# Kernel optimization log

Measured on AMD Instinct MI355X. Metric: run time of the kernel, lower is better.

Reference implementation:

```python
import jax, jax.numpy as jnp
import numpy as np

D_MODEL = 1024
NUM_HEADS = 16
D_K = D_MODEL // NUM_HEADS


def setup_inputs() -> dict:
    key = jax.random.key(0)
    ks = jax.random.split(key, 13)
    B, S = 2, 2048
    s = 1.0 / np.sqrt(D_MODEL)
    inp = {
        'q': jax.random.normal(ks[0], (B, S, D_MODEL), jnp.float32),
        'k': jax.random.normal(ks[1], (B, S, D_MODEL), jnp.float32),
        'v': jax.random.normal(ks[2], (B, S, D_MODEL), jnp.float32),
        'mask': jax.random.randint(ks[3], (B, S), 0, 2, jnp.int32),
        'Wq': jax.random.normal(ks[4], (D_MODEL, D_MODEL), jnp.float32) * s,
        'bq': jax.random.normal(ks[5], (D_MODEL,), jnp.float32) * s,
        'Wk': jax.random.normal(ks[6], (D_MODEL, D_MODEL), jnp.float32) * s,
        'bk': jax.random.normal(ks[7], (D_MODEL,), jnp.float32) * s,
        'Wv': jax.random.normal(ks[8], (D_MODEL, D_MODEL), jnp.float32) * s,
        'bv': jax.random.normal(ks[9], (D_MODEL,), jnp.float32) * s,
        'Wo': jax.random.normal(ks[10], (D_MODEL, D_MODEL), jnp.float32) * s,
        'bo': jax.random.normal(ks[11], (D_MODEL,), jnp.float32) * s,
    }
    return inp


def reference(q, k, v, mask, Wq, bq, Wk, bk, Wv, bv, Wo, bo):
    B, S, _ = q.shape

    def split(x):  # [B,S,D] -> [B,H,S,d_k]
        return x.reshape(B, -1, NUM_HEADS, D_K).transpose(0, 2, 1, 3)

    qh = split(q @ Wq.T + bq)
    kh = split(k @ Wk.T + bk)
    vh = split(v @ Wv.T + bv)

    scores = jnp.einsum('bhqd,bhkd->bhqk', qh, kh) / jnp.sqrt(jnp.float32(D_K))
    scores = jnp.where(mask[:, None, None, :] == 0, jnp.float32(-1e9), scores)
    attn = jax.nn.softmax(scores, axis=-1)
    out = jnp.einsum('bhqk,bhkd->bhqd', attn, vh)  # [B,H,S,d_k]
    out = out.transpose(0, 2, 1, 3).reshape(B, S, NUM_HEADS * D_K)
    return out @ Wo.T + bo
```

## Files before the change

kernel.cpp:

```cpp
#include <hip/hip_runtime.h>
#include <cstdint>
#include <cstddef>


using bf16   = __bf16;
using bf16x4 = __attribute__((ext_vector_type(4))) __bf16;
using bf16x8 = __attribute__((ext_vector_type(8))) __bf16;
using f32x4  = __attribute__((ext_vector_type(4))) float;

#define MFMA_BF16(a, b, c) __builtin_amdgcn_mfma_f32_16x16x32_bf16((a), (b), (c), 0, 0, 0)

__device__ __forceinline__ void gload_lds16(const void* g, void* l) {
  __builtin_amdgcn_global_load_lds((__attribute__((address_space(1))) void*)g,
                                   (__attribute__((address_space(3))) void*)l,
                                   16, 0, 0);
}

#define LOG2E 1.4426950408889634f

__global__ __launch_bounds__(256) void prep_kernel(
    const float* __restrict__ q, const float* __restrict__ k, const float* __restrict__ v,
    const int* __restrict__ mask,
    const float* __restrict__ Wq, const float* __restrict__ Wk,
    const float* __restrict__ Wv, const float* __restrict__ Wo,
    bf16* __restrict__ qb, bf16* __restrict__ kb, bf16* __restrict__ vb,
    bf16* __restrict__ Wqb, bf16* __restrict__ Wkb, bf16* __restrict__ Wvb,
    bf16* __restrict__ Wob, float* __restrict__ maskf)
{
  const int NQ = 1048576;
  const int NW = 262144;
  int i = blockIdx.x * 256 + threadIdx.x;
  if (i < 3 * NQ) {
    const float* src; bf16* dst; int j;
    if (i < NQ)        { src = q; dst = qb; j = i; }
    else if (i < 2*NQ) { src = k; dst = kb; j = i - NQ; }
    else               { src = v; dst = vb; j = i - 2*NQ; }
    float4 f = ((const float4*)src)[j];
    ((bf16x4*)dst)[j] = bf16x4{(bf16)f.x, (bf16)f.y, (bf16)f.z, (bf16)f.w};
  } else if (i < 3*NQ + 4*NW) {
    int j = i - 3*NQ;
    const float* src; bf16* dst;
    if (j < NW)        { src = Wq; dst = Wqb; }
    else if (j < 2*NW) { src = Wk; dst = Wkb; j -= NW; }
    else if (j < 3*NW) { src = Wv; dst = Wvb; j -= 2*NW; }
    else               { src = Wo; dst = Wob; j -= 3*NW; }
    float4 f = ((const float4*)src)[j];
    ((bf16x4*)dst)[j] = bf16x4{(bf16)f.x, (bf16)f.y, (bf16)f.z, (bf16)f.w};
  } else if (i < 3*NQ + 4*NW + 1024) {
    int j = i - 3*NQ - 4*NW;
    int4 mi = ((const int4*)mask)[j];
    float4 o;
    o.x = (mi.x == 0) ? -1e9f * LOG2E : 0.0f;
    o.y = (mi.y == 0) ? -1e9f * LOG2E : 0.0f;
    o.z = (mi.z == 0) ? -1e9f * LOG2E : 0.0f;
    o.w = (mi.w == 0) ? -1e9f * LOG2E : 0.0f;
    ((float4*)maskf)[j] = o;
  }
}

__global__ __launch_bounds__(256, 2) void proj3_kernel(
    const bf16* __restrict__ Xq, const bf16* __restrict__ Xk, const bf16* __restrict__ Xv,
    const bf16* __restrict__ Wqb, const bf16* __restrict__ Wkb, const bf16* __restrict__ Wvb,
    const float* __restrict__ bq, const float* __restrict__ bk, const float* __restrict__ bv,
    bf16* __restrict__ qh, bf16* __restrict__ kh, bf16* __restrict__ vhT)
{
  __shared__ bf16 As[256 * 64];
  __shared__ bf16 Bs[128 * 64];

  const int bid = blockIdx.x;
  const int z   = bid >> 7;
  const int r_  = bid & 127;

  const int tid = threadIdx.x, w = tid >> 6, lane = tid & 63;
  const int quad = lane >> 4, l16 = lane & 15;
  const int sw = l16 & 7;
  const int srow8 = lane >> 3;
  const int scol  = ((lane & 7) ^ srow8) * 8;

  const bf16* Aptr; const bf16* Bptr;
  int m0, n0;
  if (z == 2) { Aptr = Wvb; Bptr = Xv; m0 = (r_ >> 5) * 256; n0 = (r_ & 31) * 128; }
  else        { Aptr = (z == 0) ? Xq : Xk; Bptr = (z == 0) ? Wqb : Wkb;
                m0 = (r_ >> 3) * 256; n0 = (r_ & 7) * 128; }

  f32x4 acc[4][8];
#pragma unroll
  for (int mt = 0; mt < 4; ++mt)
#pragma unroll
    for (int nt = 0; nt < 8; ++nt)
      acc[mt][nt] = f32x4{0.f, 0.f, 0.f, 0.f};

  for (int k0 = 0; k0 < 1024; k0 += 64) {
#pragma unroll
    for (int c12 = 0; c12 < 12; ++c12) {
      const int c = w * 12 + c12;
      if (c < 32) {
        const int row = c * 8 + srow8;
        gload_lds16(Aptr + (size_t)(m0 + row) * 1024 + k0 + scol, As + c * 512);
      } else {
        const int cB = c - 32;
        const int row = cB * 8 + srow8;
        gload_lds16(Bptr + (size_t)(n0 + row) * 1024 + k0 + scol, Bs + cB * 512);
      }
    }
    __syncthreads();
#pragma unroll
    for (int kk = 0; kk < 2; ++kk) {
      bf16x8 af[4], bf[8];
#pragma unroll
      for (int mt = 0; mt < 4; ++mt)
        af[mt] = *(const bf16x8*)(As + (w*64 + mt*16 + l16) * 64 + ((kk*4 + quad) ^ sw) * 8);
#pragma unroll
      for (int nt = 0; nt < 8; ++nt)
        bf[nt] = *(const bf16x8*)(Bs + (nt*16 + l16) * 64 + ((kk*4 + quad) ^ sw) * 8);
#pragma unroll
      for (int mt = 0; mt < 4; ++mt)
#pragma unroll
        for (int nt = 0; nt < 8; ++nt)
          acc[mt][nt] = MFMA_BF16(af[mt], bf[nt], acc[mt][nt]);
    }
    __syncthreads();
  }

  if (z == 2) {
#pragma unroll
    for (int mt = 0; mt < 4; ++mt) {
      const int dvb = m0 + w*64 + mt*16 + quad*4;
      const float4 bv4 = *(const float4*)(bv + dvb);
#pragma unroll
      for (int nt = 0; nt < 8; ++nt) {
        const int tok = n0 + nt*16 + l16;
        const int bb = tok >> 11, s = tok & 2047;
#pragma unroll
        for (int r = 0; r < 4; ++r) {
          const int dv = dvb + r;
          const int h = dv >> 6, d = dv & 63;
          vhT[(((size_t)bb*16 + h)*64 + d)*2048 + s] = (bf16)(acc[mt][nt][r] + (&bv4.x)[r]);
        }
      }
    }
  } else {
    const float* bias = (z == 0) ? bq : bk;
#pragma unroll
    for (int mt = 0; mt < 4; ++mt) {
#pragma unroll
      for (int nt = 0; nt < 8; ++nt) {
        const int n = n0 + nt*16 + l16;
        const int h = n >> 6, d = n & 63;
        const float bn = bias[n];
#pragma unroll
        for (int r = 0; r < 4; ++r) {
          const int m  = m0 + w*64 + mt*16 + quad*4 + r;
          const int bb = m >> 11, s = m & 2047;
          const float val = acc[mt][nt][r] + bn;
          if (z == 0)
            qh[(((size_t)bb*16 + h)*2048 + s)*64 + d] = (bf16)(val * (0.125f * LOG2E));
          else
            kh[(((size_t)bb*16 + h)*2048 + s)*64 + d] = (bf16)val;
        }
      }
    }
  }
}

#define PSTRIDE 72

__global__ __launch_bounds__(256, 2) void attn_kernel(
    const bf16* __restrict__ qh, const bf16* __restrict__ kh,
    const bf16* __restrict__ vhT, const float* __restrict__ maskf,
    bf16* __restrict__ out)
{
  __shared__ bf16 Ks[2][64 * 64];
  __shared__ bf16 Vs[2][64 * 64];
  __shared__ bf16 Ps[4][16 * PSTRIDE];

  const int tid = threadIdx.x, w = tid >> 6, lane = tid & 63;
  const int quad = lane >> 4, l16 = lane & 15;
  const int sw = l16 & 7;
  const int srow8 = lane >> 3;
  const int scol  = ((lane & 7) ^ srow8) * 8;

  const int L  = blockIdx.x;
  const int bh = (L & 7) + ((L >> 7) << 3);
  const int qt = (L >> 3) & 15;
  const int b  = bh >> 4, h = bh & 15;
  const int q0 = qt * 128 + w * 32;

  const bf16* kbase = kh  + (size_t)bh * 2048 * 64;
  const bf16* vbase = vhT + (size_t)bh * 64 * 2048;
  const bf16* qbase = qh  + ((size_t)bh * 2048 + q0) * 64;
  const float* mbase = maskf + (size_t)b * 2048;
  bf16* Pw = Ps[w];

  bf16x8 aQ[2][2];
#pragma unroll
  for (int rb = 0; rb < 2; ++rb)
#pragma unroll
    for (int kk = 0; kk < 2; ++kk)
      aQ[rb][kk] = *(const bf16x8*)(qbase + (size_t)(rb*16 + l16)*64 + kk*32 + quad*8);

  f32x4 Oacc[2][4];
  float lsum[2] = {0.f, 0.f};
#pragma unroll
  for (int rb = 0; rb < 2; ++rb)
#pragma unroll
    for (int mb = 0; mb < 4; ++mb) Oacc[rb][mb] = f32x4{0.f,0.f,0.f,0.f};

  auto stage = [&](int t, int buf) {
    const int kt0 = t * 64;
#pragma unroll
    for (int c2 = 0; c2 < 2; ++c2) {
      const int c   = w * 2 + c2;
      const int row = c * 8 + srow8;
      gload_lds16(kbase + (size_t)(kt0 + row) * 64 + scol, &Ks[buf][c * 512]);
      gload_lds16(vbase + (size_t)row * 2048 + kt0 + scol, &Vs[buf][c * 512]);
    }
  };

  stage(0, 0);
  float4 mk[4], mkn[4];
#pragma unroll
  for (int mb = 0; mb < 4; ++mb)
    mk[mb] = *(const float4*)(mbase + mb*16 + quad*4);

  for (int t = 0; t < 32; ++t) {
    const int cur = t & 1;
    __syncthreads();

    if (t < 31) {
      stage(t + 1, cur ^ 1);
      const int kt0n = (t + 1) * 64;
#pragma unroll
      for (int mb = 0; mb < 4; ++mb)
        mkn[mb] = *(const float4*)(mbase + kt0n + mb*16 + quad*4);
    }

    bf16x8 fK[8], fV[8];
#pragma unroll
    for (int mb = 0; mb < 4; ++mb)
#pragma unroll
      for (int kk = 0; kk < 2; ++kk) {
        const int off = (mb*16 + l16)*64 + ((kk*4 + quad) ^ sw)*8;
        fK[mb*2+kk] = *(const bf16x8*)(&Ks[cur][off]);
        fV[mb*2+kk] = *(const bf16x8*)(&Vs[cur][off]);
      }

#pragma unroll
    for (int rb = 0; rb < 2; ++rb) {
      f32x4 sac[4];
#pragma unroll
      for (int mb = 0; mb < 4; ++mb)
        sac[mb] = f32x4{mk[mb].x, mk[mb].y, mk[mb].z, mk[mb].w};
#pragma unroll
      for (int kk = 0; kk < 2; ++kk)
#pragma unroll
        for (int mb = 0; mb < 4; ++mb)
          sac[mb] = MFMA_BF16(fK[mb*2+kk], aQ[rb][kk], sac[mb]);

      float p[4][4];
#pragma unroll
      for (int mb = 0; mb < 4; ++mb)
#pragma unroll
        for (int r = 0; r < 4; ++r) {
          p[mb][r] = exp2f(sac[mb][r]);
          lsum[rb] += p[mb][r];
        }

#pragma unroll
      for (int mb = 0; mb < 4; ++mb) {
        bf16x4 pk = bf16x4{(bf16)p[mb][0], (bf16)p[mb][1], (bf16)p[mb][2], (bf16)p[mb][3]};
        *(bf16x4*)(Pw + l16*PSTRIDE + mb*16 + quad*4) = pk;
      }
#pragma unroll
      for (int kk = 0; kk < 2; ++kk) {
        bf16x8 aP = *(const bf16x8*)(Pw + l16*PSTRIDE + kk*32 + quad*8);
#pragma unroll
        for (int mb = 0; mb < 4; ++mb)
          Oacc[rb][mb] = MFMA_BF16(fV[mb*2+kk], aP, Oacc[rb][mb]);
      }
    }

#pragma unroll
    for (int mb = 0; mb < 4; ++mb) mk[mb] = mkn[mb];
  }

#pragma unroll
  for (int rb = 0; rb < 2; ++rb) {
    float l_ = lsum[rb];
    l_ += __shfl_xor(l_, 16);
    l_ += __shfl_xor(l_, 32);
    const float inv = 1.0f / l_;
#pragma unroll
    for (int mb = 0; mb < 4; ++mb) {
      bf16x4 o = bf16x4{(bf16)(Oacc[rb][mb][0]*inv), (bf16)(Oacc[rb][mb][1]*inv),
                        (bf16)(Oacc[rb][mb][2]*inv), (bf16)(Oacc[rb][mb][3]*inv)};
      *(bf16x4*)(out + ((size_t)b*2048 + q0 + rb*16 + l16)*1024 + h*64 + mb*16 + quad*4) = o;
    }
  }
}

__global__ __launch_bounds__(256) void oproj_kernel(
    const bf16* __restrict__ Ain, const bf16* __restrict__ Wob,
    const float* __restrict__ bo, float* __restrict__ out)
{
  __shared__ bf16 As[64 * 64];
  __shared__ bf16 Bs[128 * 64];
  const int m0 = blockIdx.x * 64, n0 = blockIdx.y * 128;

  const int tid = threadIdx.x, w = tid >> 6, lane = tid & 63;
  const int quad = lane >> 4, l16 = lane & 15;
  const int sw = l16 & 7;
  const int srow8 = lane >> 3;
  const int scol  = ((lane & 7) ^ srow8) * 8;

  f32x4 acc[4][2];
#pragma unroll
  for (int mt = 0; mt < 4; ++mt)
#pragma unroll
    for (int nt = 0; nt < 2; ++nt)
      acc[mt][nt] = f32x4{0.f, 0.f, 0.f, 0.f};

  for (int k0 = 0; k0 < 1024; k0 += 64) {
#pragma unroll
    for (int c4 = 0; c4 < 6; ++c4) {
      const int c = w * 6 + c4;
      if (c < 8) {
        const int row = c * 8 + srow8;
        gload_lds16(Ain + (size_t)(m0 + row) * 1024 + k0 + scol, As + c * 512);
      } else {
        const int cB = c - 8;
        const int row = cB * 8 + srow8;
        gload_lds16(Wob + (size_t)(n0 + row) * 1024 + k0 + scol, Bs + cB * 512);
      }
    }
    __syncthreads();
#pragma unroll
    for (int kk = 0; kk < 2; ++kk) {
      bf16x8 af[4], bfr[2];
#pragma unroll
      for (int mt = 0; mt < 4; ++mt)
        af[mt] = *(const bf16x8*)(As + (mt*16 + l16) * 64 + ((kk*4 + quad) ^ sw) * 8);
#pragma unroll
      for (int nt = 0; nt < 2; ++nt)
        bfr[nt] = *(const bf16x8*)(Bs + (w*32 + nt*16 + l16) * 64 + ((kk*4 + quad) ^ sw) * 8);
#pragma unroll
      for (int mt = 0; mt < 4; ++mt)
#pragma unroll
        for (int nt = 0; nt < 2; ++nt)
          acc[mt][nt] = MFMA_BF16(af[mt], bfr[nt], acc[mt][nt]);
    }
    __syncthreads();
  }

#pragma unroll
  for (int mt = 0; mt < 4; ++mt) {
#pragma unroll
    for (int nt = 0; nt < 2; ++nt) {
      const int n = n0 + w*32 + nt*16 + l16;
      const float bn = bo[n];
#pragma unroll
      for (int r = 0; r < 4; ++r) {
        const int m = m0 + mt*16 + quad*4 + r;
        out[(size_t)m * 1024 + n] = acc[mt][nt][r] + bn;
      }
    }
  }
}

extern "C" void kernel_launch(void* const* d_in, const int* in_sizes, int n_in,
                              void* d_out, int out_size, void* d_ws, size_t ws_size,
                              hipStream_t stream)
{
  const float* q    = (const float*)d_in[0];
  const float* k    = (const float*)d_in[1];
  const float* v    = (const float*)d_in[2];
  const int*   mask = (const int*)d_in[3];
  const float* Wq   = (const float*)d_in[4];
  const float* bq   = (const float*)d_in[5];
  const float* Wk   = (const float*)d_in[6];
  const float* bk   = (const float*)d_in[7];
  const float* Wv   = (const float*)d_in[8];
  const float* bv   = (const float*)d_in[9];
  const float* Wo   = (const float*)d_in[10];
  const float* bo   = (const float*)d_in[11];

  char* ws = (char*)d_ws;
  bf16*  qb    = (bf16*)(ws);
  bf16*  kb    = (bf16*)(ws + (8ull  << 20));
  bf16*  vb    = (bf16*)(ws + (16ull << 20));
  bf16*  Wqb   = (bf16*)(ws + (24ull << 20));
  bf16*  Wkb   = (bf16*)(ws + (26ull << 20));
  bf16*  Wvb   = (bf16*)(ws + (28ull << 20));
  bf16*  Wob   = (bf16*)(ws + (30ull << 20));
  float* maskf = (float*)(ws + (32ull << 20));
  bf16*  qh    = (bf16*)(ws + (33ull << 20));
  bf16*  kh    = (bf16*)(ws + (41ull << 20));
  bf16*  vhT   = (bf16*)(ws + (49ull << 20));
  bf16*  ao    = (bf16*)(ws);
  float* out   = (float*)d_out;

  prep_kernel<<<16388, 256, 0, stream>>>(q, k, v, mask, Wq, Wk, Wv, Wo,
                                         qb, kb, vb, Wqb, Wkb, Wvb, Wob, maskf);
  proj3_kernel<<<384, 256, 0, stream>>>(qb, kb, vb, Wqb, Wkb, Wvb,
                                        bq, bk, bv, qh, kh, vhT);
  attn_kernel<<<512, 256, 0, stream>>>(qh, kh, vhT, maskf, ao);
  oproj_kernel<<<dim3(64, 8), 256, 0, stream>>>(ao, Wob, bo, out);
}
```

Baseline: 236.1 us.

## Triple-buffer K/V tiles and prefetch next K fragments into registers

The attention loop now uses a three-stage LDS ring for K/V tiles, staging tile t+2 while computing tile t, with one barrier per iteration at the end. K fragments for the next tile are preloaded into registers, with the loop unrolled by two so the register sets alternate. P uses separate per-row-block LDS buffers, exp2 uses the hardware builtin, and row sums accumulate as vectors. The goal is to hide global and LDS latency behind MFMA work, at the cost of more LDS (48KB plus P buffers) and more registers, which may reduce occupancy at 2 blocks per CU.

```diff
diff --git a/kernel.cpp b/kernel.cpp
--- a/kernel.cpp
+++ b/kernel.cpp
@@ -165,14 +165,74 @@
 
 #define PSTRIDE 72
 
+#define ATTN_BODY(T, FKC, FKN, MKC, MKN)                                        \
+  {                                                                             \
+    if ((T) < 30) stageTo((T) + 2, kvnn);                                       \
+    if ((T) < 31) {                                                             \
+      _Pragma("unroll")                                                         \
+      for (int mb = 0; mb < 4; ++mb)                                            \
+        MKN[mb] = *(const float4*)(mbase + ((T) + 1) * 64 + mb * 16);           \
+      const char* pA = kvb + kvnxt + laneA;                                     \
+      const char* pB = kvb + kvnxt + laneB;                                     \
+      _Pragma("unroll")                                                         \
+      for (int mb = 0; mb < 4; ++mb) {                                          \
+        FKN[mb*2+0] = *(const bf16x8*)(pA + mb*2048);                           \
+        FKN[mb*2+1] = *(const bf16x8*)(pB + mb*2048);                           \
+      }                                                                         \
+    }                                                                           \
+    bf16x8 fV[8];                                                               \
+    {                                                                           \
+      const char* pA = kvb + kvcur + 8192 + laneA;                              \
+      const char* pB = kvb + kvcur + 8192 + laneB;                              \
+      _Pragma("unroll")                                                         \
+      for (int mb = 0; mb < 4; ++mb) {                                          \
+        fV[mb*2+0] = *(const bf16x8*)(pA + mb*2048);                            \
+        fV[mb*2+1] = *(const bf16x8*)(pB + mb*2048);                            \
+      }                                                                         \
+    }                                                                           \
+    _Pragma("unroll")                                                           \
+    for (int rb = 0; rb < 2; ++rb) {                                            \
+      f32x4 sac[4];                                                             \
+      _Pragma("unroll")                                                         \
+      for (int mb = 0; mb < 4; ++mb)                                            \
+        sac[mb] = f32x4{MKC[mb].x, MKC[mb].y, MKC[mb].z, MKC[mb].w};            \
+      _Pragma("unroll")                                                         \
+      for (int kk = 0; kk < 2; ++kk)                                            \
+        _Pragma("unroll")                                                       \
+        for (int mb = 0; mb < 4; ++mb)                                          \
+          sac[mb] = MFMA_BF16(FKC[mb*2+kk], aQ[rb][kk], sac[mb]);               \
+      float p[4][4];                                                            \
+      _Pragma("unroll")                                                         \
+      for (int mb = 0; mb < 4; ++mb) {                                          \
+        _Pragma("unroll")                                                       \
+        for (int r = 0; r < 4; ++r) p[mb][r] = __builtin_amdgcn_exp2f(sac[mb][r]); \
+        lacc[rb] += f32x4{p[mb][0], p[mb][1], p[mb][2], p[mb][3]};              \
+      }                                                                         \
+      bf16* bWr = rb ? bW1 : bW0;                                               \
+      const bf16* bRr = rb ? bR1 : bR0;                                         \
+      _Pragma("unroll")                                                         \
+      for (int mb = 0; mb < 4; ++mb)                                            \
+        *(bf16x4*)(bWr + mb*16) = bf16x4{(bf16)p[mb][0], (bf16)p[mb][1],        \
+                                         (bf16)p[mb][2], (bf16)p[mb][3]};       \
+      _Pragma("unroll")                                                         \
+      for (int kk = 0; kk < 2; ++kk) {                                          \
+        bf16x8 aP = *(const bf16x8*)(bRr + kk*32);                              \
+        _Pragma("unroll")                                                       \
+        for (int mb = 0; mb < 4; ++mb)                                          \
+          Oacc[rb][mb] = MFMA_BF16(fV[mb*2+kk], aP, Oacc[rb][mb]);              \
+      }                                                                         \
+    }                                                                           \
+    __syncthreads();                                                            \
+    { int tmp_ = kvcur; kvcur = kvnxt; kvnxt = kvnn; kvnn = tmp_; }             \
+  }
+
 __global__ __launch_bounds__(256, 2) void attn_kernel(
     const bf16* __restrict__ qh, const bf16* __restrict__ kh,
     const bf16* __restrict__ vhT, const float* __restrict__ maskf,
     bf16* __restrict__ out)
 {
-  __shared__ bf16 Ks[2][64 * 64];
-  __shared__ bf16 Vs[2][64 * 64];
-  __shared__ bf16 Ps[4][16 * PSTRIDE];
+  __shared__ bf16 KV[3][2][4096];
+  __shared__ bf16 Ps[4][2][16 * PSTRIDE];
 
   const int tid = threadIdx.x, w = tid >> 6, lane = tid & 63;
   const int quad = lane >> 4, l16 = lane & 15;
@@ -189,104 +249,72 @@
   const bf16* kbase = kh  + (size_t)bh * 2048 * 64;
   const bf16* vbase = vhT + (size_t)bh * 64 * 2048;
   const bf16* qbase = qh  + ((size_t)bh * 2048 + q0) * 64;
-  const float* mbase = maskf + (size_t)b * 2048;
-  bf16* Pw = Ps[w];
-
-  bf16x8 aQ[2][2];
-#pragma unroll
-  for (int rb = 0; rb < 2; ++rb)
-#pragma unroll
-    for (int kk = 0; kk < 2; ++kk)
-      aQ[rb][kk] = *(const bf16x8*)(qbase + (size_t)(rb*16 + l16)*64 + kk*32 + quad*8);
-
-  f32x4 Oacc[2][4];
-  float lsum[2] = {0.f, 0.f};
-#pragma unroll
-  for (int rb = 0; rb < 2; ++rb)
-#pragma unroll
-    for (int mb = 0; mb < 4; ++mb) Oacc[rb][mb] = f32x4{0.f,0.f,0.f,0.f};
-
-  auto stage = [&](int t, int buf) {
+  const float* mbase = maskf + (size_t)b * 2048 + quad * 4;
+
+  char* kvb = (char*)&KV[0][0][0];
+
+  auto stageTo = [&](int t, int bufoff) {
     const int kt0 = t * 64;
 #pragma unroll
     for (int c2 = 0; c2 < 2; ++c2) {
       const int c   = w * 2 + c2;
       const int row = c * 8 + srow8;
-      gload_lds16(kbase + (size_t)(kt0 + row) * 64 + scol, &Ks[buf][c * 512]);
-      gload_lds16(vbase + (size_t)row * 2048 + kt0 + scol, &Vs[buf][c * 512]);
+      gload_lds16(kbase + (size_t)(kt0 + row) * 64 + scol, kvb + bufoff + c * 1024);
+      gload_lds16(vbase + (size_t)row * 2048 + kt0 + scol, kvb + bufoff + 8192 + c * 1024);
     }
   };
 
-  stage(0, 0);
-  float4 mk[4], mkn[4];
-#pragma unroll
-  for (int mb = 0; mb < 4; ++mb)
-    mk[mb] = *(const float4*)(mbase + mb*16 + quad*4);
-
-  for (int t = 0; t < 32; ++t) {
-    const int cur = t & 1;
-    __syncthreads();
-
-    if (t < 31) {
-      stage(t + 1, cur ^ 1);
-      const int kt0n = (t + 1) * 64;
-#pragma unroll
-      for (int mb = 0; mb < 4; ++mb)
-        mkn[mb] = *(const float4*)(mbase + kt0n + mb*16 + quad*4);
-    }
-
-    bf16x8 fK[8], fV[8];
-#pragma unroll
-    for (int mb = 0; mb < 4; ++mb)
-#pragma unroll
-      for (int kk = 0; kk < 2; ++kk) {
-        const int off = (mb*16 + l16)*64 + ((kk*4 + quad) ^ sw)*8;
-        fK[mb*2+kk] = *(const bf16x8*)(&Ks[cur][off]);
-        fV[mb*2+kk] = *(const bf16x8*)(&Vs[cur][off]);
-      }
-
-#pragma unroll
-    for (int rb = 0; rb < 2; ++rb) {
-      f32x4 sac[4];
-#pragma unroll
-      for (int mb = 0; mb < 4; ++mb)
-        sac[mb] = f32x4{mk[mb].x, mk[mb].y, mk[mb].z, mk[mb].w};
-#pragma unroll
-      for (int kk = 0; kk < 2; ++kk)
-#pragma unroll
-        for (int mb = 0; mb < 4; ++mb)
-          sac[mb] = MFMA_BF16(fK[mb*2+kk], aQ[rb][kk], sac[mb]);
-
-      float p[4][4];
-#pragma unroll
-      for (int mb = 0; mb < 4; ++mb)
-#pragma unroll
-        for (int r = 0; r < 4; ++r) {
-          p[mb][r] = exp2f(sac[mb][r]);
-          lsum[rb] += p[mb][r];
-        }
-
-#pragma unroll
-      for (int mb = 0; mb < 4; ++mb) {
-        bf16x4 pk = bf16x4{(bf16)p[mb][0], (bf16)p[mb][1], (bf16)p[mb][2], (bf16)p[mb][3]};
-        *(bf16x4*)(Pw + l16*PSTRIDE + mb*16 + quad*4) = pk;
-      }
-#pragma unroll
-      for (int kk = 0; kk < 2; ++kk) {
-        bf16x8 aP = *(const bf16x8*)(Pw + l16*PSTRIDE + kk*32 + quad*8);
-#pragma unroll
-        for (int mb = 0; mb < 4; ++mb)
-          Oacc[rb][mb] = MFMA_BF16(fV[mb*2+kk], aP, Oacc[rb][mb]);
-      }
-    }
-
-#pragma unroll
-    for (int mb = 0; mb < 4; ++mb) mk[mb] = mkn[mb];
-  }
-
+  bf16x8 aQ[2][2];
+#pragma unroll
+  for (int rb = 0; rb < 2; ++rb)
+#pragma unroll
+    for (int kk = 0; kk < 2; ++kk)
+      aQ[rb][kk] = *(const bf16x8*)(qbase + (size_t)(rb*16 + l16)*64 + kk*32 + quad*8);
+
+  const int laneA = l16 * 128 + ((quad    ) ^ sw) * 16;
+  const int laneB = l16 * 128 + ((quad + 4) ^ sw) * 16;
+  bf16*       bW0 = &Ps[w][0][0] + l16 * PSTRIDE + quad * 4;
+  const bf16* bR0 = &Ps[w][0][0] + l16 * PSTRIDE + quad * 8;
+  bf16*       bW1 = &Ps[w][1][0] + l16 * PSTRIDE + quad * 4;
+  const bf16* bR1 = &Ps[w][1][0] + l16 * PSTRIDE + quad * 8;
+
+  f32x4 Oacc[2][4];
+  f32x4 lacc[2];
 #pragma unroll
   for (int rb = 0; rb < 2; ++rb) {
-    float l_ = lsum[rb];
+    lacc[rb] = f32x4{0.f, 0.f, 0.f, 0.f};
+#pragma unroll
+    for (int mb = 0; mb < 4; ++mb) Oacc[rb][mb] = f32x4{0.f, 0.f, 0.f, 0.f};
+  }
+
+  stageTo(0, 0);
+  stageTo(1, 16384);
+  float4 mkA[4], mkB[4];
+#pragma unroll
+  for (int mb = 0; mb < 4; ++mb) mkA[mb] = *(const float4*)(mbase + mb*16);
+  __syncthreads();
+
+  bf16x8 fKa[8], fKb[8];
+  {
+    const char* pA = kvb + laneA;
+    const char* pB = kvb + laneB;
+#pragma unroll
+    for (int mb = 0; mb < 4; ++mb) {
+      fKa[mb*2+0] = *(const bf16x8*)(pA + mb*2048);
+      fKa[mb*2+1] = *(const bf16x8*)(pB + mb*2048);
+    }
+  }
+
+  int kvcur = 0, kvnxt = 16384, kvnn = 32768;
+
+  for (int tt = 0; tt < 32; tt += 2) {
+    ATTN_BODY(tt,     fKa, fKb, mkA, mkB);
+    ATTN_BODY(tt + 1, fKb, fKa, mkB, mkA);
+  }
+
+#pragma unroll
+  for (int rb = 0; rb < 2; ++rb) {
+    float l_ = lacc[rb][0] + lacc[rb][1] + lacc[rb][2] + lacc[rb][3];
     l_ += __shfl_xor(l_, 16);
     l_ += __shfl_xor(l_, 32);
     const float inv = 1.0f / l_;
```

Measured after the change: 222.7 us. 1.06x faster.

## Retile QKV projection to 128x128 and deepen attention K/V pipeline with larger query tiles

Applied to the files above, without the earlier changes.

The QKV projection moves from 256x128 to 128x128 tiles with a 2x2 wave layout, doubling the grid to 768 blocks and allowing 3 blocks per CU. The attention kernel now gives each wave 64 query rows (256 per block, 256 blocks), reusing each K/V tile across more queries. K/V staging becomes triple-buffered, prefetching two tiles ahead with a single barrier per iteration. It also uses the raw exp2 builtin and vector row-sum accumulation. The cost is more registers per wave in attention and only 256 attention blocks, which may underfill the GPU's CUs.

```diff
diff --git a/kernel.cpp b/kernel.cpp
--- a/kernel.cpp
+++ b/kernel.cpp
@@ -58,20 +58,21 @@
   }
 }
 
-__global__ __launch_bounds__(256, 2) void proj3_kernel(
+__global__ __launch_bounds__(256, 3) void proj3_kernel(
     const bf16* __restrict__ Xq, const bf16* __restrict__ Xk, const bf16* __restrict__ Xv,
     const bf16* __restrict__ Wqb, const bf16* __restrict__ Wkb, const bf16* __restrict__ Wvb,
     const float* __restrict__ bq, const float* __restrict__ bk, const float* __restrict__ bv,
     bf16* __restrict__ qh, bf16* __restrict__ kh, bf16* __restrict__ vhT)
 {
-  __shared__ bf16 As[256 * 64];
+  __shared__ bf16 As[128 * 64];
   __shared__ bf16 Bs[128 * 64];
 
   const int bid = blockIdx.x;
-  const int z   = bid >> 7;
-  const int r_  = bid & 127;
+  const int z   = bid >> 8;
+  const int r_  = bid & 255;
 
   const int tid = threadIdx.x, w = tid >> 6, lane = tid & 63;
+  const int wr = w >> 1, wc = w & 1;
   const int quad = lane >> 4, l16 = lane & 15;
   const int sw = l16 & 7;
   const int srow8 = lane >> 3;
@@ -79,26 +80,26 @@
 
   const bf16* Aptr; const bf16* Bptr;
   int m0, n0;
-  if (z == 2) { Aptr = Wvb; Bptr = Xv; m0 = (r_ >> 5) * 256; n0 = (r_ & 31) * 128; }
+  if (z == 2) { Aptr = Wvb; Bptr = Xv; m0 = (r_ >> 5) * 128; n0 = (r_ & 31) * 128; }
   else        { Aptr = (z == 0) ? Xq : Xk; Bptr = (z == 0) ? Wqb : Wkb;
-                m0 = (r_ >> 3) * 256; n0 = (r_ & 7) * 128; }
-
-  f32x4 acc[4][8];
+                m0 = (r_ >> 3) * 128; n0 = (r_ & 7) * 128; }
+
+  f32x4 acc[4][4];
 #pragma unroll
   for (int mt = 0; mt < 4; ++mt)
 #pragma unroll
-    for (int nt = 0; nt < 8; ++nt)
+    for (int nt = 0; nt < 4; ++nt)
       acc[mt][nt] = f32x4{0.f, 0.f, 0.f, 0.f};
 
   for (int k0 = 0; k0 < 1024; k0 += 64) {
 #pragma unroll
-    for (int c12 = 0; c12 < 12; ++c12) {
-      const int c = w * 12 + c12;
-      if (c < 32) {
+    for (int c8 = 0; c8 < 8; ++c8) {
+      const int c = w * 8 + c8;
+      if (c < 16) {
         const int row = c * 8 + srow8;
         gload_lds16(Aptr + (size_t)(m0 + row) * 1024 + k0 + scol, As + c * 512);
       } else {
-        const int cB = c - 32;
+        const int cB = c - 16;
         const int row = cB * 8 + srow8;
         gload_lds16(Bptr + (size_t)(n0 + row) * 1024 + k0 + scol, Bs + cB * 512);
       }
@@ -106,17 +107,17 @@
     __syncthreads();
 #pragma unroll
     for (int kk = 0; kk < 2; ++kk) {
-      bf16x8 af[4], bf[8];
+      bf16x8 af[4], bf[4];
 #pragma unroll
       for (int mt = 0; mt < 4; ++mt)
-        af[mt] = *(const bf16x8*)(As + (w*64 + mt*16 + l16) * 64 + ((kk*4 + quad) ^ sw) * 8);
-#pragma unroll
-      for (int nt = 0; nt < 8; ++nt)
-        bf[nt] = *(const bf16x8*)(Bs + (nt*16 + l16) * 64 + ((kk*4 + quad) ^ sw) * 8);
+        af[mt] = *(const bf16x8*)(As + (wr*64 + mt*16 + l16) * 64 + ((kk*4 + quad) ^ sw) * 8);
+#pragma unroll
+      for (int nt = 0; nt < 4; ++nt)
+        bf[nt] = *(const bf16x8*)(Bs + (wc*64 + nt*16 + l16) * 64 + ((kk*4 + quad) ^ sw) * 8);
 #pragma unroll
       for (int mt = 0; mt < 4; ++mt)
 #pragma unroll
-        for (int nt = 0; nt < 8; ++nt)
+        for (int nt = 0; nt < 4; ++nt)
           acc[mt][nt] = MFMA_BF16(af[mt], bf[nt], acc[mt][nt]);
     }
     __syncthreads();
@@ -125,11 +126,11 @@
   if (z == 2) {
 #pragma unroll
     for (int mt = 0; mt < 4; ++mt) {
-      const int dvb = m0 + w*64 + mt*16 + quad*4;
+      const int dvb = m0 + wr*64 + mt*16 + quad*4;
       const float4 bv4 = *(const float4*)(bv + dvb);
 #pragma unroll
-      for (int nt = 0; nt < 8; ++nt) {
-        const int tok = n0 + nt*16 + l16;
+      for (int nt = 0; nt < 4; ++nt) {
+        const int tok = n0 + wc*64 + nt*16 + l16;
         const int bb = tok >> 11, s = tok & 2047;
 #pragma unroll
         for (int r = 0; r < 4; ++r) {
@@ -144,13 +145,13 @@
 #pragma unroll
     for (int mt = 0; mt < 4; ++mt) {
 #pragma unroll
-      for (int nt = 0; nt < 8; ++nt) {
-        const int n = n0 + nt*16 + l16;
+      for (int nt = 0; nt < 4; ++nt) {
+        const int n = n0 + wc*64 + nt*16 + l16;
         const int h = n >> 6, d = n & 63;
         const float bn = bias[n];
 #pragma unroll
         for (int r = 0; r < 4; ++r) {
-          const int m  = m0 + w*64 + mt*16 + quad*4 + r;
+          const int m  = m0 + wr*64 + mt*16 + quad*4 + r;
           const int bb = m >> 11, s = m & 2047;
           const float val = acc[mt][nt][r] + bn;
           if (z == 0)
@@ -165,13 +166,12 @@
 
 #define PSTRIDE 72
 
-__global__ __launch_bounds__(256, 2) void attn_kernel(
+__global__ __launch_bounds__(256, 1) void attn_kernel(
     const bf16* __restrict__ qh, const bf16* __restrict__ kh,
     const bf16* __restrict__ vhT, const float* __restrict__ maskf,
     bf16* __restrict__ out)
 {
-  __shared__ bf16 Ks[2][64 * 64];
-  __shared__ bf16 Vs[2][64 * 64];
+  __shared__ bf16 KV[3][2][4096];
   __shared__ bf16 Ps[4][16 * PSTRIDE];
 
   const int tid = threadIdx.x, w = tid >> 6, lane = tid & 63;
@@ -181,72 +181,87 @@
   const int scol  = ((lane & 7) ^ srow8) * 8;
 
   const int L  = blockIdx.x;
-  const int bh = (L & 7) + ((L >> 7) << 3);
-  const int qt = (L >> 3) & 15;
+  const int bh = (L & 7) + ((L >> 6) << 3);
+  const int qt = (L >> 3) & 7;
   const int b  = bh >> 4, h = bh & 15;
-  const int q0 = qt * 128 + w * 32;
+  const int q0 = qt * 256 + w * 64;
 
   const bf16* kbase = kh  + (size_t)bh * 2048 * 64;
   const bf16* vbase = vhT + (size_t)bh * 64 * 2048;
   const bf16* qbase = qh  + ((size_t)bh * 2048 + q0) * 64;
-  const float* mbase = maskf + (size_t)b * 2048;
+  const float* mbase = maskf + (size_t)b * 2048 + quad * 4;
+
+  char* kvb = (char*)&KV[0][0][0];
   bf16* Pw = Ps[w];
 
-  bf16x8 aQ[2][2];
-#pragma unroll
-  for (int rb = 0; rb < 2; ++rb)
-#pragma unroll
-    for (int kk = 0; kk < 2; ++kk)
-      aQ[rb][kk] = *(const bf16x8*)(qbase + (size_t)(rb*16 + l16)*64 + kk*32 + quad*8);
-
-  f32x4 Oacc[2][4];
-  float lsum[2] = {0.f, 0.f};
-#pragma unroll
-  for (int rb = 0; rb < 2; ++rb)
-#pragma unroll
-    for (int mb = 0; mb < 4; ++mb) Oacc[rb][mb] = f32x4{0.f,0.f,0.f,0.f};
-
-  auto stage = [&](int t, int buf) {
+  auto stageTo = [&](int t, int bufoff) {
     const int kt0 = t * 64;
 #pragma unroll
     for (int c2 = 0; c2 < 2; ++c2) {
       const int c   = w * 2 + c2;
       const int row = c * 8 + srow8;
-      gload_lds16(kbase + (size_t)(kt0 + row) * 64 + scol, &Ks[buf][c * 512]);
-      gload_lds16(vbase + (size_t)row * 2048 + kt0 + scol, &Vs[buf][c * 512]);
+      gload_lds16(kbase + (size_t)(kt0 + row) * 64 + scol, kvb + bufoff + c * 1024);
+      gload_lds16(vbase + (size_t)row * 2048 + kt0 + scol, kvb + bufoff + 8192 + c * 1024);
     }
   };
 
-  stage(0, 0);
+  bf16x8 aQ[4][2];
+#pragma unroll
+  for (int rb = 0; rb < 4; ++rb)
+#pragma unroll
+    for (int kk = 0; kk < 2; ++kk)
+      aQ[rb][kk] = *(const bf16x8*)(qbase + (size_t)(rb*16 + l16)*64 + kk*32 + quad*8);
+
+  const int laneA = l16 * 128 + ((quad    ) ^ sw) * 16;
+  const int laneB = l16 * 128 + ((quad + 4) ^ sw) * 16;
+  bf16*       bW = Pw + l16 * PSTRIDE + quad * 4;
+  const bf16* bR = Pw + l16 * PSTRIDE + quad * 8;
+
+  f32x4 Oacc[4][4];
+  f32x4 lacc[4];
+#pragma unroll
+  for (int rb = 0; rb < 4; ++rb) {
+    lacc[rb] = f32x4{0.f, 0.f, 0.f, 0.f};
+#pragma unroll
+    for (int mb = 0; mb < 4; ++mb) Oacc[rb][mb] = f32x4{0.f, 0.f, 0.f, 0.f};
+  }
+
+  stageTo(0, 0);
+  stageTo(1, 16384);
   float4 mk[4], mkn[4];
 #pragma unroll
-  for (int mb = 0; mb < 4; ++mb)
-    mk[mb] = *(const float4*)(mbase + mb*16 + quad*4);
+  for (int mb = 0; mb < 4; ++mb) mk[mb] = *(const float4*)(mbase + mb*16);
+  __syncthreads();
+
+  int kvcur = 0, kvnxt = 16384, kvnn = 32768;
 
   for (int t = 0; t < 32; ++t) {
-    const int cur = t & 1;
-    __syncthreads();
-
+    if (t < 30) stageTo(t + 2, kvnn);
     if (t < 31) {
-      stage(t + 1, cur ^ 1);
-      const int kt0n = (t + 1) * 64;
 #pragma unroll
       for (int mb = 0; mb < 4; ++mb)
-        mkn[mb] = *(const float4*)(mbase + kt0n + mb*16 + quad*4);
+        mkn[mb] = *(const float4*)(mbase + (t + 1)*64 + mb*16);
     }
 
     bf16x8 fK[8], fV[8];
-#pragma unroll
-    for (int mb = 0; mb < 4; ++mb)
-#pragma unroll
-      for (int kk = 0; kk < 2; ++kk) {
-        const int off = (mb*16 + l16)*64 + ((kk*4 + quad) ^ sw)*8;
-        fK[mb*2+kk] = *(const bf16x8*)(&Ks[cur][off]);
-        fV[mb*2+kk] = *(const bf16x8*)(&Vs[cur][off]);
-      }
-
-#pragma unroll
-    for (int rb = 0; rb < 2; ++rb) {
+    {
+      const char* pA = kvb + kvcur + laneA;
+      const char* pB = kvb + kvcur + laneB;
+#pragma unroll
+      for (int mb = 0; mb < 4; ++mb) {
+        fK[mb*2+0] = *(const bf16x8*)(pA + mb*2048);
+        fK[mb*2+1] = *(const bf16x8*)(pB + mb*2048);
+      }
+      pA += 8192; pB += 8192;
+#pragma unroll
+      for (int mb = 0; mb < 4; ++mb) {
+        fV[mb*2+0] = *(const bf16x8*)(pA + mb*2048);
+        fV[mb*2+1] = *(const bf16x8*)(pB + mb*2048);
+      }
+    }
+
+#pragma unroll
+    for (int rb = 0; rb < 4; ++rb) {
       f32x4 sac[4];
 #pragma unroll
       for (int mb = 0; mb < 4; ++mb)
@@ -259,21 +274,20 @@
 
       float p[4][4];
 #pragma unroll
-      for (int mb = 0; mb < 4; ++mb)
-#pragma unroll
-        for (int r = 0; r < 4; ++r) {
-          p[mb][r] = exp2f(sac[mb][r]);
-          lsum[rb] += p[mb][r];
-        }
+      for (int mb = 0; mb < 4; ++mb) {
+#pragma unroll
+        for (int r = 0; r < 4; ++r) p[mb][r] = __builtin_amdgcn_exp2f(sac[mb][r]);
+        lacc[rb] += f32x4{p[mb][0], p[mb][1], p[mb][2], p[mb][3]};
+      }
 
 #pragma unroll
       for (int mb = 0; mb < 4; ++mb) {
         bf16x4 pk = bf16x4{(bf16)p[mb][0], (bf16)p[mb][1], (bf16)p[mb][2], (bf16)p[mb][3]};
-        *(bf16x4*)(Pw + l16*PSTRIDE + mb*16 + quad*4) = pk;
+        *(bf16x4*)(bW + mb*16) = pk;
       }
 #pragma unroll
       for (int kk = 0; kk < 2; ++kk) {
-        bf16x8 aP = *(const bf16x8*)(Pw + l16*PSTRIDE + kk*32 + quad*8);
+        bf16x8 aP = *(const bf16x8*)(bR + kk*32);
 #pragma unroll
         for (int mb = 0; mb < 4; ++mb)
           Oacc[rb][mb] = MFMA_BF16(fV[mb*2+kk], aP, Oacc[rb][mb]);
@@ -282,11 +296,14 @@
 
 #pragma unroll
     for (int mb = 0; mb < 4; ++mb) mk[mb] = mkn[mb];
-  }
-
-#pragma unroll
-  for (int rb = 0; rb < 2; ++rb) {
-    float l_ = lsum[rb];
+
+    __syncthreads();
+    int tmp_ = kvcur; kvcur = kvnxt; kvnxt = kvnn; kvnn = tmp_;
+  }
+
+#pragma unroll
+  for (int rb = 0; rb < 4; ++rb) {
+    float l_ = lacc[rb][0] + lacc[rb][1] + lacc[rb][2] + lacc[rb][3];
     l_ += __shfl_xor(l_, 16);
     l_ += __shfl_xor(l_, 32);
     const float inv = 1.0f / l_;
@@ -401,8 +418,8 @@
 
   prep_kernel<<<16388, 256, 0, stream>>>(q, k, v, mask, Wq, Wk, Wv, Wo,
                                          qb, kb, vb, Wqb, Wkb, Wvb, Wob, maskf);
-  proj3_kernel<<<384, 256, 0, stream>>>(qb, kb, vb, Wqb, Wkb, Wvb,
+  proj3_kernel<<<768, 256, 0, stream>>>(qb, kb, vb, Wqb, Wkb, Wvb,
                                         bq, bk, bv, qh, kh, vhT);
-  attn_kernel<<<512, 256, 0, stream>>>(qh, kh, vhT, maskf, ao);
+  attn_kernel<<<256, 256, 0, stream>>>(qh, kh, vhT, maskf, ao);
   oproj_kernel<<<dim3(64, 8), 256, 0, stream>>>(ao, Wob, bo, out);
 }
```

Result: no change. 236.0 us (-0.1%).
